# Performance work log

Measured on AMD Instinct MI355X. Metric: run time of the kernel, lower is better.

Reference implementation:

```python
import jax, jax.numpy as jnp
import numpy as np

B, S, D, H = 8, 2048, 1024, 64

def setup_inputs() -> dict:
    key = jax.random.key(0)
    ks = jax.random.split(key, 7)
    scale = 0.02
    return {
        "x": jax.random.normal(ks[0], (B, S, D), dtype=jnp.float32),
        "Wq": jax.random.normal(ks[1], (D, H), dtype=jnp.float32) * scale,
        "bq": jax.random.normal(ks[2], (H,), dtype=jnp.float32) * scale,
        "Wk": jax.random.normal(ks[3], (D, H), dtype=jnp.float32) * scale,
        "bk": jax.random.normal(ks[4], (H,), dtype=jnp.float32) * scale,
        "Wv": jax.random.normal(ks[5], (D, H), dtype=jnp.float32) * scale,
        "bv": jax.random.normal(ks[6], (H,), dtype=jnp.float32) * scale,
    }

def reference(x, Wq, bq, Wk, bk, Wv, bv):
    # Single-head causal self-attention (dropout in eval mode -> identity).
    q = x @ Wq + bq            # [B,S,H]
    k = x @ Wk + bk            # [B,S,H]
    v = x @ Wv + bv            # [B,S,H]
    scores = jnp.einsum("bqh,bkh->bqk", q, k)  # [B,S,S]
    s = q.shape[1]
    causal = jnp.tril(jnp.ones((s, s), dtype=bool))
    # Original masks with -inf BEFORE scaling; -inf/scale == -inf, so equivalent.
    scores = jnp.where(causal, scores, -jnp.inf) / jnp.sqrt(jnp.float32(k.shape[-1]))
    attn = jax.nn.softmax(scores, axis=-1)
    return jnp.einsum("bqk,bkh->bqh", attn, v)
```

## Files before the change

### kernel.cpp

```cpp
#include <hip/hip_runtime.h>
#include <math.h>

#define BATCH 8
#define SEQ   2048
#define DIM   1024
#define HD    64
#define NROWS (BATCH * SEQ)
#define CHUNK 512
#define NCHUNK 4
#define QTILE 128
#define NQT   (SEQ / QTILE)
#define QSCALE 0.1803368801f

typedef __attribute__((ext_vector_type(8))) short bf16x8;
typedef __attribute__((ext_vector_type(4))) float f32x4;

__device__ __forceinline__ unsigned short f2bf(float f) {
    unsigned u = __float_as_uint(f);
    u = (u + 0x7FFFu + ((u >> 16) & 1u)) >> 16;
    return (unsigned short)u;
}
__device__ __forceinline__ unsigned short f2bf_hu(float f) {
    return (unsigned short)((__float_as_uint(f) + 0x8000u) >> 16);
}
__device__ __forceinline__ float fast_exp2(float x) {
#if __has_builtin(__builtin_amdgcn_exp2f)
    return __builtin_amdgcn_exp2f(x);
#else
    return exp2f(x);
#endif
}

__device__ __forceinline__ void gld_lds16(const void* g, void* l) {
    __builtin_amdgcn_global_load_lds(
        (const __attribute__((address_space(1))) void*)g,
        (__attribute__((address_space(3))) void*)l, 16, 0, 0);
}

__device__ __forceinline__ uint4 pack_bf16x8(float4 a, float4 b) {
    uint4 o;
    o.x = ((__float_as_uint(a.x) + 0x8000u) >> 16) | ((__float_as_uint(a.y) + 0x8000u) & 0xFFFF0000u);
    o.y = ((__float_as_uint(a.z) + 0x8000u) >> 16) | ((__float_as_uint(a.w) + 0x8000u) & 0xFFFF0000u);
    o.z = ((__float_as_uint(b.x) + 0x8000u) >> 16) | ((__float_as_uint(b.y) + 0x8000u) & 0xFFFF0000u);
    o.w = ((__float_as_uint(b.z) + 0x8000u) >> 16) | ((__float_as_uint(b.w) + 0x8000u) & 0xFFFF0000u);
    return o;
}

#define CFENCE() asm volatile("" ::: "memory")
#define RAW_BAR() do { CFENCE(); __builtin_amdgcn_s_barrier(); CFENCE(); } while (0)

__global__ __launch_bounds__(256)
void prep_w_kernel(const float* __restrict__ Wq, const float* __restrict__ Wk,
                   const float* __restrict__ Wv, unsigned short* __restrict__ Wt)
{
    const int mat = blockIdx.y;
    const float* __restrict__ W = (mat == 0) ? Wq : (mat == 1) ? Wk : Wv;
    const int k0 = blockIdx.x * 64;
    __shared__ float T[64][65];
    const int t = threadIdx.x;
    #pragma unroll
    for (int i = 0; i < 16; ++i) {
        const int idx = t + i * 256;
        T[idx >> 6][idx & 63] = W[(size_t)(k0 + (idx >> 6)) * HD + (idx & 63)];
    }
    __syncthreads();
    const int n = t >> 2;
    const int c = t & 3;
    union { unsigned short h[16]; uint4 v[2]; } buf;
    #pragma unroll
    for (int j = 0; j < 16; ++j) buf.h[j] = f2bf(T[c * 16 + j][n]);
    unsigned short* dst = Wt + ((size_t)mat * HD + n) * DIM + k0 + c * 16;
    *(uint4*)dst       = buf.v[0];
    *(uint4*)(dst + 8) = buf.v[1];
}

__global__ __launch_bounds__(768)
void qkv_mfma_kernel(const float* __restrict__ x,
                     const unsigned short* __restrict__ Wt,
                     const float* __restrict__ bq, const float* __restrict__ bk,
                     const float* __restrict__ bv,
                     unsigned short* __restrict__ Qg,
                     unsigned short* __restrict__ Kg,
                     unsigned short* __restrict__ Vtg)
{
    __shared__ unsigned short Xs[2][64][64];
    __shared__ unsigned short Ws[2][192][64];

    const int t    = threadIdx.x;
    const int lane = t & 63;
    const int w    = t >> 6;
    const int col  = lane & 15;
    const int quad = lane >> 4;
    const int mat  = w >> 2;
    const int wr   = w & 3;
    const int row0 = blockIdx.x * 64;

    const int r8  = lane >> 3;
    const int ch8 = lane & 7;
    const int wswz = (ch8 ^ r8) * 8;

    f32x4 acc[4];
    #pragma unroll
    for (int i = 0; i < 4; ++i) acc[i] = (f32x4){0.f, 0.f, 0.f, 0.f};

    const int xr  = t >> 3;
    const int xc0 = t & 7;
    const float* __restrict__ xrow = &x[(size_t)(row0 + xr) * DIM];

    auto stageW = [&](int it, int bb) {
        const int k0 = it * 64;
        #pragma unroll
        for (int ii = 0; ii < 2; ++ii) {
            const int rbase = w * 16 + ii * 8;
            gld_lds16(&Wt[(size_t)(rbase + r8) * DIM + k0 + wswz], &Ws[bb][rbase][0]);
        }
    };
    auto computeT = [&](int bb) {
        #pragma unroll
        for (int ks = 0; ks < 2; ++ks) {
            const int fswz = ((ks * 4 + quad) ^ (col & 7)) * 8;
            const bf16x8 a = *(const bf16x8*)&Xs[bb][wr * 16 + col][fswz];
            #pragma unroll
            for (int nt = 0; nt < 4; ++nt) {
                const bf16x8 b = *(const bf16x8*)&Ws[bb][mat * 64 + nt * 16 + col][fswz];
                acc[nt] = __builtin_amdgcn_mfma_f32_16x16x32_bf16(a, b, acc[nt], 0, 0, 0);
            }
        }
    };

    float4 xa, xb;
    stageW(0, 0);
    if (t < 512) {
        xa = *(const float4*)(xrow + xc0 * 8);
        xb = *(const float4*)(xrow + xc0 * 8 + 4);
    }
    asm volatile("s_waitcnt vmcnt(0)" ::: "memory");
    if (t < 512) {
        *(uint4*)&Xs[0][xr][(xc0 ^ (xr & 7)) * 8] = pack_bf16x8(xa, xb);
        xa = *(const float4*)(xrow + 64 + xc0 * 8);
        xb = *(const float4*)(xrow + 64 + xc0 * 8 + 4);
    }

    int buf = 0;
    for (int it = 0; it < 16; ++it) {
        RAW_BAR();
        if (it < 15) {
            stageW(it + 1, buf ^ 1);
            asm volatile("s_waitcnt vmcnt(2)" ::: "memory");
            if (t < 512) {
                *(uint4*)&Xs[buf ^ 1][xr][(xc0 ^ (xr & 7)) * 8] = pack_bf16x8(xa, xb);
                if (it < 14) {
                    const float* xp = xrow + (it + 2) * 64;
                    xa = *(const float4*)(xp + xc0 * 8);
                    xb = *(const float4*)(xp + xc0 * 8 + 4);
                }
            }
        } else {
            asm volatile("s_waitcnt vmcnt(0)" ::: "memory");
        }
        RAW_BAR();
        computeT(buf);
        buf ^= 1;
    }

    const int b    = row0 / SEQ;
    const int s0   = (row0 % SEQ) + wr * 16 + quad * 4;
    const int grow = row0 + wr * 16 + quad * 4;
    const float* __restrict__ bias = (mat == 0) ? bq : (mat == 1) ? bk : bv;
    const float oscale = (mat == 0) ? QSCALE : 1.0f;
    #pragma unroll
    for (int nt = 0; nt < 4; ++nt) {
        const int nn = nt * 16 + col;
        const float bvv = bias[nn];
        if (mat < 2) {
            unsigned short* __restrict__ o = (mat == 0) ? Qg : Kg;
            #pragma unroll
            for (int r = 0; r < 4; ++r)
                o[(size_t)(grow + r) * HD + nn] = f2bf((acc[nt][r] + bvv) * oscale);
        } else {
            const unsigned lo = (unsigned)f2bf(acc[nt][0] + bvv) | ((unsigned)f2bf(acc[nt][1] + bvv) << 16);
            const unsigned hi = (unsigned)f2bf(acc[nt][2] + bvv) | ((unsigned)f2bf(acc[nt][3] + bvv) << 16);
            *(uint2*)&Vtg[((size_t)b * HD + nn) * SEQ + s0] = make_uint2(lo, hi);
        }
    }
}

__global__ __launch_bounds__(512)
void attn_part_kernel(const unsigned short* __restrict__ Qg,
                      const unsigned short* __restrict__ Kg,
                      const unsigned short* __restrict__ Vtg,
                      unsigned short* __restrict__ Opart,
                      float* __restrict__ Lsum)
{
    const int b = blockIdx.x;
    int y = blockIdx.y, c = 0;
    while (y >= NQT - 4 * c) { y -= NQT - 4 * c; ++c; }
    const int qt = y + 4 * c;

    __shared__ unsigned short Ks[2][64][64];
    __shared__ unsigned short Vs[2][64][64];
    __shared__ unsigned short Ps[8][16][76];

    const int t    = threadIdx.x;
    const int w    = t >> 6;
    const int lane = t & 63;
    const int col  = lane & 15;
    const int quad = lane >> 4;
    const int q0w  = qt * QTILE + w * 16;
    const size_t gq = (size_t)b * SEQ + q0w;

    const bf16x8 aq0 = *(const bf16x8*)&Qg[(gq + col) * HD + quad * 8];
    const bf16x8 aq1 = *(const bf16x8*)&Qg[(gq + col) * HD + 32 + quad * 8];

    f32x4 oacc[4];
    #pragma unroll
    for (int n = 0; n < 4; ++n) oacc[n] = (f32x4){0.f, 0.f, 0.f, 0.f};
    float lpart[4] = {0.f, 0.f, 0.f, 0.f};

    const int kbeg   = c * CHUNK;
    const int kend   = min((c + 1) * CHUNK, (qt + 1) * QTILE);
    const int ntiles = (kend - kbeg + 63) >> 6;

    const int r8 = lane >> 3, ch = lane & 7;
    const int swzr = (ch ^ r8) * 8;
    const unsigned short* kgb = Kg  + (size_t)b * SEQ * HD;
    const unsigned short* vgb = Vtg + (size_t)b * HD * SEQ;

    auto stageKV = [&](int it, int bb) {
        const int j0 = kbeg + it * 64;
        const int rb = w * 8;
        gld_lds16(&kgb[(size_t)(j0 + rb + r8) * HD + swzr], &Ks[bb][rb][0]);
        gld_lds16(&vgb[(size_t)(rb + r8) * SEQ + j0 + swzr], &Vs[bb][rb][0]);
    };

    stageKV(0, 0);

    int bufb = 0;
    for (int it = 0; it < ntiles; ++it) {
        RAW_BAR();
        if (it + 1 < ntiles) {
            stageKV(it + 1, bufb ^ 1);
            asm volatile("s_waitcnt vmcnt(2)" ::: "memory");
        } else {
            asm volatile("s_waitcnt vmcnt(0)" ::: "memory");
        }
        RAW_BAR();
        const int j0 = kbeg + it * 64;

        if (j0 <= q0w + 15) {
            f32x4 scv[4];
            #pragma unroll
            for (int nt = 0; nt < 4; ++nt) {
                const int sw0 = (quad ^ (col & 7)) * 8;
                const int sw1 = ((4 + quad) ^ (col & 7)) * 8;
                const bf16x8 bk0 = *(const bf16x8*)&Ks[bufb][nt * 16 + col][sw0];
                const bf16x8 bk1 = *(const bf16x8*)&Ks[bufb][nt * 16 + col][sw1];
                f32x4 s = __builtin_amdgcn_mfma_f32_16x16x32_bf16(aq0, bk0, (f32x4){0.f,0.f,0.f,0.f}, 0, 0, 0);
                s = __builtin_amdgcn_mfma_f32_16x16x32_bf16(aq1, bk1, s, 0, 0, 0);
                scv[nt] = s;
            }
            const bool needmask = (j0 + 63 > q0w);
            #pragma unroll
            for (int r = 0; r < 4; ++r) {
                const int row = q0w + quad * 4 + r;
                #pragma unroll
                for (int nt = 0; nt < 4; ++nt) {
                    float s = scv[nt][r];
                    if (needmask)
                        s = (j0 + nt * 16 + col <= row) ? s : -INFINITY;
                    const float p = fast_exp2(s);
                    lpart[r] += p;
                    Ps[w][quad * 4 + r][nt * 16 + col] = f2bf_hu(p);
                }
            }
            #pragma unroll
            for (int ks = 0; ks < 2; ++ks) {
                const bf16x8 ap = *(const bf16x8*)&Ps[w][col][ks * 32 + quad * 8];
                const int fswz = ((ks * 4 + quad) ^ (col & 7)) * 8;
                #pragma unroll
                for (int n = 0; n < 4; ++n) {
                    const bf16x8 bv2 = *(const bf16x8*)&Vs[bufb][n * 16 + col][fswz];
                    oacc[n] = __builtin_amdgcn_mfma_f32_16x16x32_bf16(ap, bv2, oacc[n], 0, 0, 0);
                }
            }
        }
        bufb ^= 1;
    }

    #pragma unroll
    for (int r = 0; r < 4; ++r) {
        #pragma unroll
        for (int off = 1; off < 16; off <<= 1)
            lpart[r] += __shfl_xor(lpart[r], off, 64);
    }

    const int blk = (b * NQT + qt) * NCHUNK + c;
    unsigned short* Ob = Opart + (size_t)blk * (QTILE * HD);
    #pragma unroll
    for (int n = 0; n < 4; ++n)
        #pragma unroll
        for (int r = 0; r < 4; ++r)
            Ob[(w * 16 + quad * 4 + r) * HD + n * 16 + col] = f2bf(oacc[n][r]);
    if (col == 0) {
        float* lb = Lsum + (size_t)blk * QTILE + w * 16;
        #pragma unroll
        for (int r = 0; r < 4; ++r)
            lb[quad * 4 + r] = lpart[r];
    }
}

__global__ __launch_bounds__(256)
void combine_kernel(const unsigned short* __restrict__ Opart,
                    const float* __restrict__ Lsum,
                    float* __restrict__ out)
{
    const int gid = blockIdx.x * 256 + threadIdx.x;
    const int i   = gid >> 4;
    const int d4  = (gid & 15) * 4;
    const int b   = i >> 11;
    const int s   = i & 2047;
    const int qt  = s >> 7;
    const int r   = s & 127;
    const int nc  = (s >> 9) + 1;
    const int blk0 = (b * NQT + qt) * NCHUNK;

    float L = 0.f;
    float a0 = 0.f, a1 = 0.f, a2 = 0.f, a3 = 0.f;
    for (int cc = 0; cc < nc; ++cc) {
        L += Lsum[(size_t)(blk0 + cc) * QTILE + r];
        const uint2 u = *(const uint2*)(Opart + (size_t)(blk0 + cc) * (QTILE * HD) + r * HD + d4);
        a0 += __uint_as_float(u.x << 16);
        a1 += __uint_as_float(u.x & 0xFFFF0000u);
        a2 += __uint_as_float(u.y << 16);
        a3 += __uint_as_float(u.y & 0xFFFF0000u);
    }
    const float rL = 1.0f / L;
    float4 o; o.x = a0 * rL; o.y = a1 * rL; o.z = a2 * rL; o.w = a3 * rL;
    *(float4*)&out[(size_t)i * HD + d4] = o;
}

extern "C" void kernel_launch(void* const* d_in, const int* in_sizes, int n_in,
                              void* d_out, int out_size, void* d_ws, size_t ws_size,
                              hipStream_t stream) {
    const float* x  = (const float*)d_in[0];
    const float* Wq = (const float*)d_in[1];
    const float* bq = (const float*)d_in[2];
    const float* Wk = (const float*)d_in[3];
    const float* bk = (const float*)d_in[4];
    const float* Wv = (const float*)d_in[5];
    const float* bv = (const float*)d_in[6];
    float* out = (float*)d_out;

    unsigned short* Wt    = (unsigned short*)d_ws;
    unsigned short* Qg    = Wt + (size_t)3 * HD * DIM;
    unsigned short* Kg    = Qg + (size_t)NROWS * HD;
    unsigned short* Vtg   = Kg + (size_t)NROWS * HD;
    unsigned short* Opart = Vtg + (size_t)BATCH * HD * SEQ;
    float* Lsum = (float*)(Opart + (size_t)BATCH * NQT * NCHUNK * QTILE * HD);

    prep_w_kernel<<<dim3(16, 3), 256, 0, stream>>>(Wq, Wk, Wv, Wt);
    qkv_mfma_kernel<<<dim3(NROWS / 64), 768, 0, stream>>>(x, Wt, bq, bk, bv, Qg, Kg, Vtg);
    attn_part_kernel<<<dim3(8, 40), 512, 0, stream>>>(Qg, Kg, Vtg, Opart, Lsum);
    combine_kernel<<<dim3(NROWS * 16 / 256), 256, 0, stream>>>(Opart, Lsum, out);
}
```

Measured before the change: 138.2 us.

## Replace split-K attention plus combine with single-pass 64-row query tiles

Measured after the change: 156.7 us. +13.4%, slower.

```diff
diff --git a/kernel.cpp b/kernel.cpp
--- a/kernel.cpp
+++ b/kernel.cpp
@@ -6,9 +6,7 @@
 #define DIM   1024
 #define HD    64
 #define NROWS (BATCH * SEQ)
-#define CHUNK 512
-#define NCHUNK 4
-#define QTILE 128
+#define QTILE 64
 #define NQT   (SEQ / QTILE)
 #define QSCALE 0.1803368801f
 
@@ -185,21 +183,18 @@
     }
 }
 
-__global__ __launch_bounds__(512)
-void attn_part_kernel(const unsigned short* __restrict__ Qg,
+__global__ __launch_bounds__(256)
+void attn_full_kernel(const unsigned short* __restrict__ Qg,
                       const unsigned short* __restrict__ Kg,
                       const unsigned short* __restrict__ Vtg,
-                      unsigned short* __restrict__ Opart,
-                      float* __restrict__ Lsum)
+                      float* __restrict__ out)
 {
-    const int b = blockIdx.x;
-    int y = blockIdx.y, c = 0;
-    while (y >= NQT - 4 * c) { y -= NQT - 4 * c; ++c; }
-    const int qt = y + 4 * c;
+    const int b  = blockIdx.x;
+    const int qt = blockIdx.y;
 
     __shared__ unsigned short Ks[2][64][64];
     __shared__ unsigned short Vs[2][64][64];
-    __shared__ unsigned short Ps[8][16][76];
+    __shared__ unsigned short Ps[4][16][76];
 
     const int t    = threadIdx.x;
     const int w    = t >> 6;
@@ -217,9 +212,7 @@
     for (int n = 0; n < 4; ++n) oacc[n] = (f32x4){0.f, 0.f, 0.f, 0.f};
     float lpart[4] = {0.f, 0.f, 0.f, 0.f};
 
-    const int kbeg   = c * CHUNK;
-    const int kend   = min((c + 1) * CHUNK, (qt + 1) * QTILE);
-    const int ntiles = (kend - kbeg + 63) >> 6;
+    const int ntiles = qt + 1;
 
     const int r8 = lane >> 3, ch = lane & 7;
     const int swzr = (ch ^ r8) * 8;
@@ -227,10 +220,13 @@
     const unsigned short* vgb = Vtg + (size_t)b * HD * SEQ;
 
     auto stageKV = [&](int it, int bb) {
-        const int j0 = kbeg + it * 64;
-        const int rb = w * 8;
-        gld_lds16(&kgb[(size_t)(j0 + rb + r8) * HD + swzr], &Ks[bb][rb][0]);
-        gld_lds16(&vgb[(size_t)(rb + r8) * SEQ + j0 + swzr], &Vs[bb][rb][0]);
+        const int j0 = it * 64;
+        #pragma unroll
+        for (int ii = 0; ii < 2; ++ii) {
+            const int rb = w * 16 + ii * 8;
+            gld_lds16(&kgb[(size_t)(j0 + rb + r8) * HD + swzr], &Ks[bb][rb][0]);
+            gld_lds16(&vgb[(size_t)(rb + r8) * SEQ + j0 + swzr], &Vs[bb][rb][0]);
+        }
     };
 
     stageKV(0, 0);
@@ -240,48 +236,46 @@
         RAW_BAR();
         if (it + 1 < ntiles) {
             stageKV(it + 1, bufb ^ 1);
-            asm volatile("s_waitcnt vmcnt(2)" ::: "memory");
+            asm volatile("s_waitcnt vmcnt(4)" ::: "memory");
         } else {
             asm volatile("s_waitcnt vmcnt(0)" ::: "memory");
         }
         RAW_BAR();
-        const int j0 = kbeg + it * 64;
-
-        if (j0 <= q0w + 15) {
-            f32x4 scv[4];
+        const int j0 = it * 64;
+
+        f32x4 scv[4];
+        #pragma unroll
+        for (int nt = 0; nt < 4; ++nt) {
+            const int sw0 = (quad ^ (col & 7)) * 8;
+            const int sw1 = ((4 + quad) ^ (col & 7)) * 8;
+            const bf16x8 bk0 = *(const bf16x8*)&Ks[bufb][nt * 16 + col][sw0];
+            const bf16x8 bk1 = *(const bf16x8*)&Ks[bufb][nt * 16 + col][sw1];
+            f32x4 s = __builtin_amdgcn_mfma_f32_16x16x32_bf16(aq0, bk0, (f32x4){0.f,0.f,0.f,0.f}, 0, 0, 0);
+            s = __builtin_amdgcn_mfma_f32_16x16x32_bf16(aq1, bk1, s, 0, 0, 0);
+            scv[nt] = s;
+        }
+        const bool needmask = (j0 + 63 > q0w);
+        #pragma unroll
+        for (int r = 0; r < 4; ++r) {
+            const int row = q0w + quad * 4 + r;
             #pragma unroll
             for (int nt = 0; nt < 4; ++nt) {
-                const int sw0 = (quad ^ (col & 7)) * 8;
-                const int sw1 = ((4 + quad) ^ (col & 7)) * 8;
-                const bf16x8 bk0 = *(const bf16x8*)&Ks[bufb][nt * 16 + col][sw0];
-                const bf16x8 bk1 = *(const bf16x8*)&Ks[bufb][nt * 16 + col][sw1];
-                f32x4 s = __builtin_amdgcn_mfma_f32_16x16x32_bf16(aq0, bk0, (f32x4){0.f,0.f,0.f,0.f}, 0, 0, 0);
-                s = __builtin_amdgcn_mfma_f32_16x16x32_bf16(aq1, bk1, s, 0, 0, 0);
-                scv[nt] = s;
+                float s = scv[nt][r];
+                if (needmask)
+                    s = (j0 + nt * 16 + col <= row) ? s : -INFINITY;
+                const float p = fast_exp2(s);
+                lpart[r] += p;
+                Ps[w][quad * 4 + r][nt * 16 + col] = f2bf_hu(p);
             }
-            const bool needmask = (j0 + 63 > q0w);
+        }
+        #pragma unroll
+        for (int ks = 0; ks < 2; ++ks) {
+            const bf16x8 ap = *(const bf16x8*)&Ps[w][col][ks * 32 + quad * 8];
+            const int fswz = ((ks * 4 + quad) ^ (col & 7)) * 8;
             #pragma unroll
-            for (int r = 0; r < 4; ++r) {
-                const int row = q0w + quad * 4 + r;
-                #pragma unroll
-                for (int nt = 0; nt < 4; ++nt) {
-                    float s = scv[nt][r];
-                    if (needmask)
-                        s = (j0 + nt * 16 + col <= row) ? s : -INFINITY;
-                    const float p = fast_exp2(s);
-                    lpart[r] += p;
-                    Ps[w][quad * 4 + r][nt * 16 + col] = f2bf_hu(p);
-                }
-            }
-            #pragma unroll
-            for (int ks = 0; ks < 2; ++ks) {
-                const bf16x8 ap = *(const bf16x8*)&Ps[w][col][ks * 32 + quad * 8];
-                const int fswz = ((ks * 4 + quad) ^ (col & 7)) * 8;
-                #pragma unroll
-                for (int n = 0; n < 4; ++n) {
-                    const bf16x8 bv2 = *(const bf16x8*)&Vs[bufb][n * 16 + col][fswz];
-                    oacc[n] = __builtin_amdgcn_mfma_f32_16x16x32_bf16(ap, bv2, oacc[n], 0, 0, 0);
-                }
+            for (int n = 0; n < 4; ++n) {
+                const bf16x8 bv2 = *(const bf16x8*)&Vs[bufb][n * 16 + col][fswz];
+                oacc[n] = __builtin_amdgcn_mfma_f32_16x16x32_bf16(ap, bv2, oacc[n], 0, 0, 0);
             }
         }
         bufb ^= 1;
@@ -293,50 +287,15 @@
         for (int off = 1; off < 16; off <<= 1)
             lpart[r] += __shfl_xor(lpart[r], off, 64);
     }
-
-    const int blk = (b * NQT + qt) * NCHUNK + c;
-    unsigned short* Ob = Opart + (size_t)blk * (QTILE * HD);
+    float rL[4];
+    #pragma unroll
+    for (int r = 0; r < 4; ++r) rL[r] = 1.0f / lpart[r];
+
     #pragma unroll
     for (int n = 0; n < 4; ++n)
         #pragma unroll
         for (int r = 0; r < 4; ++r)
-            Ob[(w * 16 + quad * 4 + r) * HD + n * 16 + col] = f2bf(oacc[n][r]);
-    if (col == 0) {
-        float* lb = Lsum + (size_t)blk * QTILE + w * 16;
-        #pragma unroll
-        for (int r = 0; r < 4; ++r)
-            lb[quad * 4 + r] = lpart[r];
-    }
-}
-
-__global__ __launch_bounds__(256)
-void combine_kernel(const unsigned short* __restrict__ Opart,
-                    const float* __restrict__ Lsum,
-                    float* __restrict__ out)
-{
-    const int gid = blockIdx.x * 256 + threadIdx.x;
-    const int i   = gid >> 4;
-    const int d4  = (gid & 15) * 4;
-    const int b   = i >> 11;
-    const int s   = i & 2047;
-    const int qt  = s >> 7;
-    const int r   = s & 127;
-    const int nc  = (s >> 9) + 1;
-    const int blk0 = (b * NQT + qt) * NCHUNK;
-
-    float L = 0.f;
-    float a0 = 0.f, a1 = 0.f, a2 = 0.f, a3 = 0.f;
-    for (int cc = 0; cc < nc; ++cc) {
-        L += Lsum[(size_t)(blk0 + cc) * QTILE + r];
-        const uint2 u = *(const uint2*)(Opart + (size_t)(blk0 + cc) * (QTILE * HD) + r * HD + d4);
-        a0 += __uint_as_float(u.x << 16);
-        a1 += __uint_as_float(u.x & 0xFFFF0000u);
-        a2 += __uint_as_float(u.y << 16);
-        a3 += __uint_as_float(u.y & 0xFFFF0000u);
-    }
-    const float rL = 1.0f / L;
-    float4 o; o.x = a0 * rL; o.y = a1 * rL; o.z = a2 * rL; o.w = a3 * rL;
-    *(float4*)&out[(size_t)i * HD + d4] = o;
+            out[(gq + quad * 4 + r) * HD + n * 16 + col] = oacc[n][r] * rL[r];
 }
 
 extern "C" void kernel_launch(void* const* d_in, const int* in_sizes, int n_in,
@@ -355,11 +314,8 @@
     unsigned short* Qg    = Wt + (size_t)3 * HD * DIM;
     unsigned short* Kg    = Qg + (size_t)NROWS * HD;
     unsigned short* Vtg   = Kg + (size_t)NROWS * HD;
-    unsigned short* Opart = Vtg + (size_t)BATCH * HD * SEQ;
-    float* Lsum = (float*)(Opart + (size_t)BATCH * NQT * NCHUNK * QTILE * HD);
 
     prep_w_kernel<<<dim3(16, 3), 256, 0, stream>>>(Wq, Wk, Wv, Wt);
     qkv_mfma_kernel<<<dim3(NROWS / 64), 768, 0, stream>>>(x, Wt, bq, bk, bv, Qg, Kg, Vtg);
-    attn_part_kernel<<<dim3(8, 40), 512, 0, stream>>>(Qg, Kg, Vtg, Opart, Lsum);
-    combine_kernel<<<dim3(NROWS * 16 / 256), 256, 0, stream>>>(Opart, Lsum, out);
-}
+    attn_full_kernel<<<dim3(8, NQT), 256, 0, stream>>>(Qg, Kg, Vtg, out);
+}
```

## Fuse split-K combine into attention kernel via last-block atomic counter

Applied to the files above, without the earlier changes.

Measured after the change: 233.9 us. +69.3%, slower.

```diff
diff --git a/kernel.cpp b/kernel.cpp
--- a/kernel.cpp
+++ b/kernel.cpp
@@ -49,15 +49,28 @@
 #define CFENCE() asm volatile("" ::: "memory")
 #define RAW_BAR() do { CFENCE(); __builtin_amdgcn_s_barrier(); CFENCE(); } while (0)
 
+__device__ __constant__ unsigned char ATTN_MAP[40] = {
+    12, 16, 20, 24, 28, 32, 36, 40, 44, 48, 52, 56, 60,
+    29, 33, 37, 41, 45, 49, 53, 57, 61,
+    46, 50, 54, 58, 62,
+    63,
+    8, 25, 42, 59,
+    4, 21, 38, 55,
+    0, 17, 34, 51
+};
+
 __global__ __launch_bounds__(256)
 void prep_w_kernel(const float* __restrict__ Wq, const float* __restrict__ Wk,
-                   const float* __restrict__ Wv, unsigned short* __restrict__ Wt)
+                   const float* __restrict__ Wv, unsigned short* __restrict__ Wt,
+                   unsigned* __restrict__ Cnt)
 {
     const int mat = blockIdx.y;
     const float* __restrict__ W = (mat == 0) ? Wq : (mat == 1) ? Wk : Wv;
     const int k0 = blockIdx.x * 64;
     __shared__ float T[64][65];
     const int t = threadIdx.x;
+    if (blockIdx.x == 0 && mat == 0 && t < BATCH * NQT)
+        Cnt[t] = 0u;
     #pragma unroll
     for (int i = 0; i < 16; ++i) {
         const int idx = t + i * 256;
@@ -190,16 +203,19 @@
                       const unsigned short* __restrict__ Kg,
                       const unsigned short* __restrict__ Vtg,
                       unsigned short* __restrict__ Opart,
-                      float* __restrict__ Lsum)
+                      float* __restrict__ Lsum,
+                      unsigned* __restrict__ Cnt,
+                      float* __restrict__ out)
 {
     const int b = blockIdx.x;
-    int y = blockIdx.y, c = 0;
-    while (y >= NQT - 4 * c) { y -= NQT - 4 * c; ++c; }
-    const int qt = y + 4 * c;
+    const int code = ATTN_MAP[blockIdx.y];
+    const int qt = code >> 2;
+    const int c  = code & 3;
 
     __shared__ unsigned short Ks[2][64][64];
     __shared__ unsigned short Vs[2][64][64];
     __shared__ unsigned short Ps[8][16][76];
+    __shared__ int isLast;
 
     const int t    = threadIdx.x;
     const int w    = t >> 6;
@@ -307,36 +323,44 @@
         for (int r = 0; r < 4; ++r)
             lb[quad * 4 + r] = lpart[r];
     }
-}
-
-__global__ __launch_bounds__(256)
-void combine_kernel(const unsigned short* __restrict__ Opart,
-                    const float* __restrict__ Lsum,
-                    float* __restrict__ out)
-{
-    const int gid = blockIdx.x * 256 + threadIdx.x;
-    const int i   = gid >> 4;
-    const int d4  = (gid & 15) * 4;
-    const int b   = i >> 11;
-    const int s   = i & 2047;
-    const int qt  = s >> 7;
-    const int r   = s & 127;
-    const int nc  = (s >> 9) + 1;
+
+    __threadfence();
+    __syncthreads();
+    const int nchunks = (qt >> 2) + 1;
+    if (t == 0)
+        isLast = (atomicAdd(&Cnt[b * NQT + qt], 1u) == (unsigned)(nchunks - 1));
+    __syncthreads();
+    if (!isLast) return;
+    __threadfence();
+
+    const int r   = t >> 2;
+    const int d0  = (t & 3) * 16;
     const int blk0 = (b * NQT + qt) * NCHUNK;
-
+    const size_t grow = (size_t)b * SEQ + qt * QTILE + r;
     float L = 0.f;
-    float a0 = 0.f, a1 = 0.f, a2 = 0.f, a3 = 0.f;
-    for (int cc = 0; cc < nc; ++cc) {
-        L += Lsum[(size_t)(blk0 + cc) * QTILE + r];
-        const uint2 u = *(const uint2*)(Opart + (size_t)(blk0 + cc) * (QTILE * HD) + r * HD + d4);
-        a0 += __uint_as_float(u.x << 16);
-        a1 += __uint_as_float(u.x & 0xFFFF0000u);
-        a2 += __uint_as_float(u.y << 16);
-        a3 += __uint_as_float(u.y & 0xFFFF0000u);
+    float a[16];
+    #pragma unroll
+    for (int j = 0; j < 16; ++j) a[j] = 0.f;
+    for (int cc = 0; cc < nchunks; ++cc) {
+        L += __hip_atomic_load(&Lsum[(size_t)(blk0 + cc) * QTILE + r],
+                               __ATOMIC_RELAXED, __HIP_MEMORY_SCOPE_AGENT);
+        const unsigned short* Op = Opart + (size_t)(blk0 + cc) * (QTILE * HD) + r * HD + d0;
+        #pragma unroll
+        for (int j = 0; j < 4; ++j) {
+            const unsigned long long u = __hip_atomic_load(
+                (const unsigned long long*)(Op + j * 4),
+                __ATOMIC_RELAXED, __HIP_MEMORY_SCOPE_AGENT);
+            a[j * 4 + 0] += __uint_as_float((unsigned)(u      ) << 16);
+            a[j * 4 + 1] += __uint_as_float((unsigned)(u      ) & 0xFFFF0000u);
+            a[j * 4 + 2] += __uint_as_float((unsigned)(u >> 32) << 16);
+            a[j * 4 + 3] += __uint_as_float((unsigned)(u >> 32) & 0xFFFF0000u);
+        }
     }
     const float rL = 1.0f / L;
-    float4 o; o.x = a0 * rL; o.y = a1 * rL; o.z = a2 * rL; o.w = a3 * rL;
-    *(float4*)&out[(size_t)i * HD + d4] = o;
+    float4* op = (float4*)&out[grow * HD + d0];
+    #pragma unroll
+    for (int j = 0; j < 4; ++j)
+        op[j] = (float4){a[j*4] * rL, a[j*4+1] * rL, a[j*4+2] * rL, a[j*4+3] * rL};
 }
 
 extern "C" void kernel_launch(void* const* d_in, const int* in_sizes, int n_in,
@@ -357,9 +381,9 @@
     unsigned short* Vtg   = Kg + (size_t)NROWS * HD;
     unsigned short* Opart = Vtg + (size_t)BATCH * HD * SEQ;
     float* Lsum = (float*)(Opart + (size_t)BATCH * NQT * NCHUNK * QTILE * HD);
-
-    prep_w_kernel<<<dim3(16, 3), 256, 0, stream>>>(Wq, Wk, Wv, Wt);
+    unsigned* Cnt = (unsigned*)(Lsum + (size_t)BATCH * NQT * NCHUNK * QTILE);
+
+    prep_w_kernel<<<dim3(16, 3), 256, 0, stream>>>(Wq, Wk, Wv, Wt, Cnt);
     qkv_mfma_kernel<<<dim3(NROWS / 64), 768, 0, stream>>>(x, Wt, bq, bk, bv, Qg, Kg, Vtg);
-    attn_part_kernel<<<dim3(8, 40), 512, 0, stream>>>(Qg, Kg, Vtg, Opart, Lsum);
-    combine_kernel<<<dim3(NROWS * 16 / 256), 256, 0, stream>>>(Opart, Lsum, out);
-}
+    attn_part_kernel<<<dim3(8, 40), 512, 0, stream>>>(Qg, Kg, Vtg, Opart, Lsum, Cnt, out);
+}
```
